# Optimization experiments

Measured on AMD Instinct MI355X. Metric: run time of the kernel, lower is better.

Reference implementation:

```python
import jax, jax.numpy as jnp
import numpy as np

SCORE_THRESH = 0.5
NMS_THRESH = 0.4
TOP_K = 1000  # fixed pre-NMS candidate budget (jit-safe replacement for boolean masking)
STRIDES = (8, 16, 32)
H, W = 2176, 3840


def _anchor_centers(fh, fw, stride):
    yv, xv = jnp.meshgrid(jnp.arange(fh), jnp.arange(fw), indexing='ij')
    return (jnp.stack([xv, yv], -1).reshape(-1, 2).astype(jnp.float32)) * stride  # [N,2]


def _decode_level(scores, bbox, kps, stride):
    fh, fw = H // stride, W // stride
    c = _anchor_centers(fh, fw, stride)                 # [N,2]
    s = jax.nn.sigmoid(scores.reshape(-1))              # [N]
    d = bbox.reshape(-1, 4) * stride                    # [N,4]
    boxes = jnp.concatenate([c - d[:, :2], c + d[:, 2:4]], axis=1)  # x1y1x2y2
    k = kps.reshape(-1, 5, 2) * stride + c[:, None, :]  # (x,y) pairs
    return s, boxes, k.reshape(-1, 10)


def _iou_matrix(b):
    area = (b[:, 2] - b[:, 0]) * (b[:, 3] - b[:, 1])
    lt = jnp.maximum(b[:, None, :2], b[None, :, :2])
    rb = jnp.minimum(b[:, None, 2:], b[None, :, 2:])
    wh = jnp.clip(rb - lt, 0.0)
    inter = wh[..., 0] * wh[..., 1]
    return inter / jnp.clip(area[:, None] + area[None, :] - inter, 1e-9)


def _nms_keep(iou, valid):
    n = iou.shape[0]
    ar = jnp.arange(n)

    def body(i, keep):
        sup = (iou[i] > NMS_THRESH) & (ar > i) & keep[i]
        return keep & ~sup

    return jax.lax.fori_loop(0, n, body, valid)


def reference(x, scores8, bbox8, kps8, scores16, bbox16, kps16, scores32, bbox32, kps32):
    levels = ((scores8, bbox8, kps8), (scores16, bbox16, kps16), (scores32, bbox32, kps32))
    ss, bs, ks = [], [], []
    for (s, b, k), stride in zip(levels, STRIDES):
        si, bi, ki = _decode_level(s, b, k, stride)
        ss.append(si); bs.append(bi); ks.append(ki)
    scores = jnp.concatenate(ss)   # [N_total]
    boxes = jnp.concatenate(bs)    # [N_total,4]
    kpss = jnp.concatenate(ks)     # [N_total,10]

    masked = jnp.where(scores > SCORE_THRESH, scores, -1.0)
    top_s, idx = jax.lax.top_k(masked, TOP_K)
    valid = top_s > SCORE_THRESH
    b = boxes[idx]
    k = kpss[idx]

    keep = jax.lax.stop_gradient(_nms_keep(_iou_matrix(b), valid))
    final_boxes = jnp.where(keep[:, None], b, 0.0)
    final_scores = jnp.where(keep, top_s, 0.0)
    final_kpss = jnp.where(keep[:, None], k, 0.0)
    return final_boxes, final_scores, final_kpss


def setup_inputs() -> dict:
    key = jax.random.key(0)
    ks = jax.random.split(key, 10)
    n8 = (H // 8) * (W // 8)
    n16 = (H // 16) * (W // 16)
    n32 = (H // 32) * (W // 32)
    return {
        'x': jax.random.normal(ks[0], (1, 3, H, W), jnp.float32),
        'scores8': jax.random.normal(ks[1], (1, n8, 1), jnp.float32),
        'bbox8': jax.random.uniform(ks[2], (1, n8, 4), jnp.float32),
        'kps8': jax.random.normal(ks[3], (1, n8, 10), jnp.float32),
        'scores16': jax.random.normal(ks[4], (1, n16, 1), jnp.float32),
        'bbox16': jax.random.uniform(ks[5], (1, n16, 4), jnp.float32),
        'kps16': jax.random.normal(ks[6], (1, n16, 10), jnp.float32),
        'scores32': jax.random.normal(ks[7], (1, n32, 1), jnp.float32),
        'bbox32': jax.random.uniform(ks[8], (1, n32, 4), jnp.float32),
        'kps32': jax.random.normal(ks[9], (1, n32, 10), jnp.float32),
    }
```

## Files before the change

### kernel.cpp

```cpp
#include <hip/hip_runtime.h>
#include <stdint.h>

typedef unsigned int u32;
typedef unsigned long long u64;

#define N8   130560
#define N16  32640
#define N32  8160
#define NTOT 171360
#define NTOT4 42840
#define TOPK 1000
#define NWORDS 16
#define NBINS 512
#define BUCKET_SCALE 85.25f
#define LIST_CAP 2016
#define CPB 32
#define HIST_BLKS 84
#define HIST_THR 512
#define CMP_BLKS 168
#define RANK_BLKS 63
#define IOU_BLKS 63
#define IOU_TASKS (TOPK * NWORDS)
#define NMS_CACHE 256
#define POISON 0xAAAAAAAAu


#define MI_CNT 0
#define MI_IOU 128
#define MI_ARR 256
#define MI_B   384
#define META_U32 512
#define META_ZERO 256

#define OFF_PART 0
#define OFF_META 86016
#define OFF_NZ   88064
#define OFF_LIST 88192
#define OFF_MASK 104320

__device__ __forceinline__ u32 ald32(const u32* p) {
  return __hip_atomic_load(p, __ATOMIC_RELAXED, __HIP_MEMORY_SCOPE_AGENT);
}
__device__ __forceinline__ u64 ald64(const u64* p) {
  return __hip_atomic_load(p, __ATOMIC_RELAXED, __HIP_MEMORY_SCOPE_AGENT);
}
__device__ __forceinline__ void ast32(u32* p, u32 v) {
  __hip_atomic_store(p, v, __ATOMIC_RELAXED, __HIP_MEMORY_SCOPE_AGENT);
}
__device__ __forceinline__ void ast64(u64* p, u64 v) {
  __hip_atomic_store(p, v, __ATOMIC_RELAXED, __HIP_MEMORY_SCOPE_AGENT);
}
__device__ __forceinline__ u32 normc(u32 v) {
  return v >= 0x80000000u ? v - POISON : v;
}
__device__ __forceinline__ bool arrive_last(u32* p, u32 total) {
  u32 old = __hip_atomic_fetch_add(p, 1u, __ATOMIC_RELAXED, __HIP_MEMORY_SCOPE_AGENT);
  if (normc(old) == total - 1u) { ast32(p, 0u); return true; }
  return false;
}

__device__ __forceinline__ u32 bucket_of(float x) {
  u32 b = (u32)(x * BUCKET_SCALE);
  return b > (NBINS - 1) ? (NBINS - 1) : b;
}

__device__ __forceinline__ float4 load_logit4(int v, const float* s8, const float* s16,
                                              const float* s32) {
  int e = v * 4;
  if (e < N8) return ((const float4*)s8)[v];
  if (e < N8 + N16) return ((const float4*)s16)[v - N8 / 4];
  return ((const float4*)s32)[v - (N8 + N16) / 4];
}

__device__ __forceinline__ bool iou_gt04(float4 a, float4 b) {
#pragma clang fp contract(off)
  float areaA = (a.z - a.x) * (a.w - a.y);
  float areaB = (b.z - b.x) * (b.w - b.y);
  float ltx = fmaxf(a.x, b.x);
  float lty = fmaxf(a.y, b.y);
  float rbx = fminf(a.z, b.z);
  float rby = fminf(a.w, b.w);
  float wx = rbx - ltx; wx = wx > 0.0f ? wx : 0.0f;
  float wy = rby - lty; wy = wy > 0.0f ? wy : 0.0f;
  float inter = wx * wy;
  float un = areaA + areaB - inter;
  un = un > 1e-9f ? un : 1e-9f;
  return (inter / un) > 0.4f;
}

__device__ __forceinline__ u64 valid_word(int w, u32 vcnt) {
  int lo = w * 64;
  if ((int)vcnt >= lo + 64) return ~0ull;
  if ((int)vcnt <= lo) return 0ull;
  return (1ull << (vcnt - (u32)lo)) - 1ull;
}

__global__ void __launch_bounds__(HIST_THR) k1_hist(
    const float* __restrict__ s8, const float* __restrict__ s16, const float* __restrict__ s32,
    u32* __restrict__ part, u32* meta, u64* __restrict__ nz) {
  __shared__ u32 lh[NBINS];
  __shared__ u32 csum[256];
  __shared__ int sLast;
  const int t = threadIdx.x, blk = blockIdx.x;
  lh[t < NBINS ? t : 0] = 0;
  __syncthreads();
  int v = blk * HIST_THR + t;
  if (v < NTOT4) {
    float4 x = load_logit4(v, s8, s16, s32);
    if (x.x > 0.0f) atomicAdd(&lh[bucket_of(x.x)], 1u);
    if (x.y > 0.0f) atomicAdd(&lh[bucket_of(x.y)], 1u);
    if (x.z > 0.0f) atomicAdd(&lh[bucket_of(x.z)], 1u);
    if (x.w > 0.0f) atomicAdd(&lh[bucket_of(x.w)], 1u);
  }
  __syncthreads();
  if (t < 256)
    ast32(&part[blk * 256 + t], lh[2 * t] | (lh[2 * t + 1] << 16));
  if (blk == 0) {
    if (t < META_ZERO) meta[t] = 0;
    if (t < NWORDS) nz[t] = 0ull;
  }
  __syncthreads();
  if (t == 0) sLast = arrive_last(&meta[MI_ARR], HIST_BLKS) ? 1 : 0;
  __syncthreads();
  if (!sLast) return;

  u32 lo = 0, hi = 0;
  if (t < 256) {
    int p = 0;
    for (; p + 4 <= HIST_BLKS; p += 4) {
      u32 a0 = ald32(&part[(p + 0) * 256 + t]);
      u32 a1 = ald32(&part[(p + 1) * 256 + t]);
      u32 a2 = ald32(&part[(p + 2) * 256 + t]);
      u32 a3 = ald32(&part[(p + 3) * 256 + t]);
      lo += (a0 & 0xFFFFu) + (a1 & 0xFFFFu) + (a2 & 0xFFFFu) + (a3 & 0xFFFFu);
      hi += (a0 >> 16) + (a1 >> 16) + (a2 >> 16) + (a3 >> 16);
    }
    for (; p < HIST_BLKS; ++p) {
      u32 a = ald32(&part[p * 256 + t]);
      lo += a & 0xFFFFu; hi += a >> 16;
    }
  }
  __syncthreads();
  if (t < 256) { lh[2 * t] = lo; lh[2 * t + 1] = hi; csum[t] = lo + hi; }
  __syncthreads();
  for (int off = 1; off < 256; off <<= 1) {
    u32 add = (t < 256 && t + off < 256) ? csum[t + off] : 0u;
    __syncthreads();
    if (t < 256) csum[t] += add;
    __syncthreads();
  }
  if (t == 0 && csum[0] < TOPK) meta[MI_B] = 0u;
  if (t < 256) {
    u32 above = (t < 255) ? csum[t + 1] : 0u;
    if (csum[t] >= TOPK && above < TOPK) {
      u32 cum = above + lh[2 * t + 1];
      meta[MI_B] = (cum >= TOPK) ? (u32)(2 * t + 1) : (u32)(2 * t);
    }
  }
}

__global__ void __launch_bounds__(256) k4_compact(
    const float* __restrict__ s8, const float* __restrict__ s16, const float* __restrict__ s32,
    u32* __restrict__ meta, u64* __restrict__ list) {
  __shared__ u32 sB, sBase;
  __shared__ u32 cnt16[16];
  const int t = threadIdx.x, blk = blockIdx.x;
  const int wave = t >> 6, lane = t & 63;
  const int v = blk * 256 + t;
  if (t == 0) sB = meta[MI_B];
  float4 x = make_float4(-1.f, -1.f, -1.f, -1.f);
  if (v < NTOT4) x = load_logit4(v, s8, s16, s32);
  __syncthreads();
  const u32 B = sB;
  float c[4] = {x.x, x.y, x.z, x.w};
  u32 win = 0;
#pragma unroll
  for (int j = 0; j < 4; ++j)
    if (c[j] > 0.0f && bucket_of(c[j]) >= B) win |= 1u << j;
  u32 wpos[4], wcnt[4];
#pragma unroll
  for (int j = 0; j < 4; ++j) {
    u64 bal = __ballot((win >> j) & 1u);
    wcnt[j] = (u32)__popcll(bal);
    wpos[j] = (u32)__popcll(bal & ((1ull << lane) - 1ull));
  }
  if (lane == 0) {
#pragma unroll
    for (int j = 0; j < 4; ++j) cnt16[wave * 4 + j] = wcnt[j];
  }
  __syncthreads();
  if (t == 0) {
    u32 tot = 0, pre[16];
#pragma unroll
    for (int k = 0; k < 16; ++k) { pre[k] = tot; tot += cnt16[k]; }
#pragma unroll
    for (int k = 0; k < 16; ++k) cnt16[k] = pre[k];
    sBase = tot ? atomicAdd(&meta[MI_CNT], tot) : 0u;
  }
  __syncthreads();
#pragma unroll
  for (int j = 0; j < 4; ++j) {
    if ((win >> j) & 1u) {
      u32 dst = sBase + cnt16[wave * 4 + j] + wpos[j];
      if (dst < LIST_CAP) {
        u32 idx = (u32)(v * 4 + j);
        list[dst] = ((u64)__float_as_uint(c[j]) << 32) | (u64)(~idx);
      }
    }
  }
}

__global__ void __launch_bounds__(256) k5_rank(
    const u32* __restrict__ meta, const u64* __restrict__ list,
    const float* __restrict__ bb8,  const float* __restrict__ kp8,
    const float* __restrict__ bb16, const float* __restrict__ kp16,
    const float* __restrict__ bb32, const float* __restrict__ kp32,
    float* __restrict__ out) {
  __shared__ __align__(16) u64 keys[LIST_CAP];
  __shared__ u32 rpart[256];
  __shared__ u32 sCnt;
  const int t = threadIdx.x, blk = blockIdx.x;
  if (t == 0) { u32 cc = meta[MI_CNT]; sCnt = cc > LIST_CAP ? LIST_CAP : cc; }
  __syncthreads();
  const u32 cnt = sCnt;
  for (int j = t; j < LIST_CAP; j += 256) keys[j] = (j < (int)cnt) ? list[j] : 0ull;
  __syncthreads();
  {
    const int ci = t & 31, sl = t >> 5;
    const int c = blk * CPB + ci;
    const int chunk = ((int)cnt + 7) >> 3;
    int lo = sl * chunk; if (lo > (int)cnt) lo = (int)cnt;
    int hi = lo + chunk; if (hi > (int)cnt) hi = (int)cnt;
    u64 my = keys[c];
    int r = 0, j = lo;
    for (; j + 4 <= hi; j += 4)
      r += (keys[j] > my) + (keys[j + 1] > my) + (keys[j + 2] > my) + (keys[j + 3] > my);
    for (; j < hi; ++j) r += (keys[j] > my);
    rpart[t] = (u32)r;
  }
  __syncthreads();
  if (t < CPB) {
    const int c = blk * CPB + t;
    if (c < (int)cnt) {
      int rank = 0;
#pragma unroll
      for (int q = 0; q < 8; ++q) rank += (int)rpart[t + 32 * q];
      if (rank < TOPK) {
        u64 my = keys[c];
        float lx = __uint_as_float((u32)(my >> 32));
        float sc = (float)(1.0 / (1.0 + exp(-(double)lx)));
        u32 idx = ~((u32)my);
        float4 box;
        float kv[10];
        int p, xq, yq;
        float st;
        const float *bb, *kp;
        if (idx < N8) {
          st = 8.f;  p = (int)idx;              xq = p % 480; yq = p / 480; bb = bb8;  kp = kp8;
        } else if (idx < N8 + N16) {
          st = 16.f; p = (int)idx - N8;         xq = p % 240; yq = p / 240; bb = bb16; kp = kp16;
        } else {
          st = 32.f; p = (int)idx - (N8 + N16); xq = p % 120; yq = p / 120; bb = bb32; kp = kp32;
        }
        float cx = (float)xq * st, cy = (float)yq * st;
        {
#pragma clang fp contract(off)
          float d0 = bb[4 * p + 0] * st;
          float d1 = bb[4 * p + 1] * st;
          float d2 = bb[4 * p + 2] * st;
          float d3 = bb[4 * p + 3] * st;
          box.x = cx - d0; box.y = cy - d1; box.z = cx + d2; box.w = cy + d3;
          for (int q = 0; q < 10; ++q)
            kv[q] = kp[10 * p + q] * st + ((q & 1) ? cy : cx);
        }
        ((float4*)out)[rank] = box;
        out[4000 + rank] = sc;
#pragma unroll
        for (int q = 0; q < 10; ++q) out[5000 + 10 * rank + q] = kv[q];
      }
    } else if (c < TOPK) {
      ((float4*)out)[c] = make_float4(0.f, 0.f, 0.f, 0.f);
      out[4000 + c] = 0.f;
#pragma unroll
      for (int q = 0; q < 10; ++q) out[5000 + 10 * c + q] = 0.f;
    }
  }
}

__global__ void __launch_bounds__(256) k67_iou_nms(
    u32* meta, u64* nzWords, u64* mask, float* out) {
  __shared__ __align__(16) char smem[36864];
  __shared__ int isLast;
  __shared__ u32 sPc[16], sOff17[17];
  __shared__ u64 sRem[NWORDS];
  const int t = threadIdx.x, blk = blockIdx.x;

  float4* boxes = (float4*)smem;
  for (int r = t; r < TOPK; r += 256) boxes[r] = ((const float4*)out)[r];
  __syncthreads();
  int task = blk * 256 + t;
  if (task < IOU_TASKS) {
    int w = task / 1000;
    int i = task - w * 1000;
    float4 a = boxes[i];
    int bse = w * 64;
    int jend = (bse + 64) < TOPK ? (bse + 64) : TOPK;
    u64 bits = 0;
    for (int j = bse; j < jend; ++j)
      if (j > i && iou_gt04(a, boxes[j])) bits |= 1ull << (j - bse);
    ast64(&mask[(u64)w * 1000 + i], bits);
    if (bits) atomicOr(&nzWords[i >> 6], 1ull << (i & 63));
  }
  __syncthreads();
  if (t == 0)
    isLast = (__hip_atomic_fetch_add(&meta[MI_IOU], 1u, __ATOMIC_RELAXED,
                                     __HIP_MEMORY_SCOPE_AGENT) == (u32)(IOU_BLKS - 1));
  __syncthreads();
  if (!isLast) return;

  u32 cc = meta[MI_CNT];
  if (cc > LIST_CAP) cc = LIST_CAP;
  const u32 vcnt = cc < TOPK ? cc : TOPK;
  u32* rows = (u32*)smem;
  u64* cache = (u64*)(smem + 4096);
  u64 nzv = 0;
  if (t < NWORDS) {
    nzv = ald64(&nzWords[t]) & valid_word(t, vcnt);
    sPc[t] = (u32)__popcll(nzv);
  }
  __syncthreads();
  if (t == 0) {
    u32 o = 0;
    for (int w = 0; w < NWORDS; ++w) { sOff17[w] = o; o += sPc[w]; }
    sOff17[16] = o;
  }
  __syncthreads();
  if (t < NWORDS) {
    u64 m = nzv;
    u32 o = sOff17[t];
    while (m) { int b = __builtin_ctzll(m); m &= m - 1; rows[o++] = (u32)(t * 64 + b); }
  }
  __syncthreads();
  const int S = (int)sOff17[16];
  const int Sc = S < NMS_CACHE ? S : NMS_CACHE;
  for (int idx = t; idx < Sc * NWORDS; idx += 256) {
    int s = idx >> 4, w = idx & 15;
    cache[s * NWORDS + w] = ald64(&mask[(u64)w * 1000 + rows[s]]);
  }
  __syncthreads();
  if (t < 64) {
    u64 remv = 0;
    for (int s = 0; s < S; ++s) {
      u32 row = rows[s];
      int c = (int)(row >> 6), b = (int)(row & 63);
      u64 remc = __shfl(remv, c);
      if (!((remc >> b) & 1ull)) {
        u64 m = 0;
        if (t < NWORDS)
          m = (s < NMS_CACHE) ? cache[s * NWORDS + t] : ald64(&mask[(u64)t * 1000 + row]);
        remv |= m;
      }
    }
    if (t < NWORDS) sRem[t] = valid_word(t, vcnt) & remv;
  }
  __syncthreads();
  for (int r = t; r < TOPK; r += 256) {
    if ((sRem[r >> 6] >> (r & 63)) & 1ull) {
      ((float4*)out)[r] = make_float4(0.f, 0.f, 0.f, 0.f);
      out[4000 + r] = 0.f;
#pragma unroll
      for (int q = 0; q < 10; ++q) out[5000 + 10 * r + q] = 0.f;
    }
  }
}

extern "C" void kernel_launch(void* const* d_in, const int* in_sizes, int n_in,
                              void* d_out, int out_size, void* d_ws, size_t ws_size,
                              hipStream_t stream) {
  const float* s8   = (const float*)d_in[1];
  const float* bb8  = (const float*)d_in[2];
  const float* kp8  = (const float*)d_in[3];
  const float* s16  = (const float*)d_in[4];
  const float* bb16 = (const float*)d_in[5];
  const float* kp16 = (const float*)d_in[6];
  const float* s32  = (const float*)d_in[7];
  const float* bb32 = (const float*)d_in[8];
  const float* kp32 = (const float*)d_in[9];

  char* ws = (char*)d_ws;
  u32* part    = (u32*)(ws + OFF_PART);
  u32* meta    = (u32*)(ws + OFF_META);
  u64* nzWords = (u64*)(ws + OFF_NZ);
  u64* list    = (u64*)(ws + OFF_LIST);
  u64* mask    = (u64*)(ws + OFF_MASK);
  float* out   = (float*)d_out;

  k1_hist<<<HIST_BLKS, HIST_THR, 0, stream>>>(s8, s16, s32, part, meta, nzWords);
  k4_compact<<<CMP_BLKS, 256, 0, stream>>>(s8, s16, s32, meta, list);
  k5_rank<<<RANK_BLKS, 256, 0, stream>>>(meta, list, bb8, kp8, bb16, kp16, bb32, kp32, out);
  k67_iou_nms<<<IOU_BLKS, 256, 0, stream>>>(meta, nzWords, mask, out);
}
```

Measured before the change: 169.7 us.

## Precompute per-block compaction offsets in histogram kernel, drop global atomic counter

The histogram kernel now uses 42 blocks that each cover 1024 float4s, caches the per-block partial histograms in LDS, and in the last block computes each block's count of winners above threshold bucket B together with exclusive prefix offsets. The compaction kernel uses the same 42-block partition and writes to those precomputed bases, replacing the global atomicAdd on a shared counter. This also makes list order deterministic. The IoU kernel moves to 32 blocks of 512 threads. The trade-offs are fewer blocks in the streaming kernels and more serial work in the last histogram block.

```diff
diff --git a/kernel.cpp b/kernel.cpp
--- a/kernel.cpp
+++ b/kernel.cpp
@@ -15,28 +15,29 @@
 #define BUCKET_SCALE 85.25f
 #define LIST_CAP 2016
 #define CPB 32
-#define HIST_BLKS 84
-#define HIST_THR 512
-#define CMP_BLKS 168
+#define NB1 42
+#define THR1 512
 #define RANK_BLKS 63
-#define IOU_BLKS 63
+#define IOU_BLKS 32
+#define IOU_THR 512
 #define IOU_TASKS (TOPK * NWORDS)
 #define NMS_CACHE 256
 #define POISON 0xAAAAAAAAu
 
 
-#define MI_CNT 0
-#define MI_IOU 128
-#define MI_ARR 256
-#define MI_B   384
+#define MI_IOU  0
+#define MI_ARR  128
+#define MI_B    256
+#define MI_TOT  257
+#define MI_BASE 258
 #define META_U32 512
-#define META_ZERO 256
+#define META_ZERO 128
 
 #define OFF_PART 0
-#define OFF_META 86016
-#define OFF_NZ   88064
-#define OFF_LIST 88192
-#define OFF_MASK 104320
+#define OFF_META 43008
+#define OFF_NZ   45056
+#define OFF_LIST 45184
+#define OFF_MASK 61312
 
 __device__ __forceinline__ u32 ald32(const u32* p) {
   return __hip_atomic_load(p, __ATOMIC_RELAXED, __HIP_MEMORY_SCOPE_AGENT);
@@ -95,18 +96,31 @@
   return (1ull << (vcnt - (u32)lo)) - 1ull;
 }
 
-__global__ void __launch_bounds__(HIST_THR) k1_hist(
+__global__ void __launch_bounds__(THR1) k1_hist(
     const float* __restrict__ s8, const float* __restrict__ s16, const float* __restrict__ s32,
     u32* __restrict__ part, u32* meta, u64* __restrict__ nz) {
   __shared__ u32 lh[NBINS];
+  __shared__ u32 ldsp[NB1 * 256];
   __shared__ u32 csum[256];
+  __shared__ u32 redlo[THR1], redhi[THR1];
+  __shared__ u32 red8[64][8];
+  __shared__ u32 base42[NB1 + 1];
+  __shared__ u32 sB2;
   __shared__ int sLast;
   const int t = threadIdx.x, blk = blockIdx.x;
-  lh[t < NBINS ? t : 0] = 0;
-  __syncthreads();
-  int v = blk * HIST_THR + t;
-  if (v < NTOT4) {
-    float4 x = load_logit4(v, s8, s16, s32);
+
+  if (t < NBINS) lh[t] = 0;
+  __syncthreads();
+  const int v0 = blk * 1024 + t, v1 = v0 + 512;
+  if (v0 < NTOT4) {
+    float4 x = load_logit4(v0, s8, s16, s32);
+    if (x.x > 0.0f) atomicAdd(&lh[bucket_of(x.x)], 1u);
+    if (x.y > 0.0f) atomicAdd(&lh[bucket_of(x.y)], 1u);
+    if (x.z > 0.0f) atomicAdd(&lh[bucket_of(x.z)], 1u);
+    if (x.w > 0.0f) atomicAdd(&lh[bucket_of(x.w)], 1u);
+  }
+  if (v1 < NTOT4) {
+    float4 x = load_logit4(v1, s8, s16, s32);
     if (x.x > 0.0f) atomicAdd(&lh[bucket_of(x.x)], 1u);
     if (x.y > 0.0f) atomicAdd(&lh[bucket_of(x.y)], 1u);
     if (x.z > 0.0f) atomicAdd(&lh[bucket_of(x.z)], 1u);
@@ -120,28 +134,27 @@
     if (t < NWORDS) nz[t] = 0ull;
   }
   __syncthreads();
-  if (t == 0) sLast = arrive_last(&meta[MI_ARR], HIST_BLKS) ? 1 : 0;
+  if (t == 0) sLast = arrive_last(&meta[MI_ARR], NB1) ? 1 : 0;
   __syncthreads();
   if (!sLast) return;
 
-  u32 lo = 0, hi = 0;
+  {
+    const u32 b = (u32)(t & 255);
+    u32 lo = 0, hi = 0;
+    for (int p = t >> 8; p < NB1; p += 2) {
+      u32 w = ald32(&part[p * 256 + b]);
+      ldsp[p * 256 + b] = w;
+      lo += w & 0xFFFFu; hi += w >> 16;
+    }
+    redlo[t] = lo; redhi[t] = hi;
+  }
+  __syncthreads();
+  u32 glo = 0, ghi = 0;
   if (t < 256) {
-    int p = 0;
-    for (; p + 4 <= HIST_BLKS; p += 4) {
-      u32 a0 = ald32(&part[(p + 0) * 256 + t]);
-      u32 a1 = ald32(&part[(p + 1) * 256 + t]);
-      u32 a2 = ald32(&part[(p + 2) * 256 + t]);
-      u32 a3 = ald32(&part[(p + 3) * 256 + t]);
-      lo += (a0 & 0xFFFFu) + (a1 & 0xFFFFu) + (a2 & 0xFFFFu) + (a3 & 0xFFFFu);
-      hi += (a0 >> 16) + (a1 >> 16) + (a2 >> 16) + (a3 >> 16);
-    }
-    for (; p < HIST_BLKS; ++p) {
-      u32 a = ald32(&part[p * 256 + t]);
-      lo += a & 0xFFFFu; hi += a >> 16;
-    }
-  }
-  __syncthreads();
-  if (t < 256) { lh[2 * t] = lo; lh[2 * t + 1] = hi; csum[t] = lo + hi; }
+    glo = redlo[t] + redlo[t + 256];
+    ghi = redhi[t] + redhi[t + 256];
+    csum[t] = glo + ghi;
+  }
   __syncthreads();
   for (int off = 1; off < 256; off <<= 1) {
     u32 add = (t < 256 && t + off < 256) ? csum[t + off] : 0u;
@@ -149,61 +162,86 @@
     if (t < 256) csum[t] += add;
     __syncthreads();
   }
-  if (t == 0 && csum[0] < TOPK) meta[MI_B] = 0u;
+  if (t == 0 && csum[0] < TOPK) sB2 = 0u;
   if (t < 256) {
     u32 above = (t < 255) ? csum[t + 1] : 0u;
-    if (csum[t] >= TOPK && above < TOPK) {
-      u32 cum = above + lh[2 * t + 1];
-      meta[MI_B] = (cum >= TOPK) ? (u32)(2 * t + 1) : (u32)(2 * t);
-    }
-  }
-}
-
-__global__ void __launch_bounds__(256) k4_compact(
+    if (csum[t] >= TOPK && above < TOPK)
+      sB2 = (above + ghi >= TOPK) ? (u32)(2 * t + 1) : (u32)(2 * t);
+  }
+  __syncthreads();
+  const u32 B = sB2;
+
+  {
+    const int g = t >> 3, l = t & 7;
+    u32 acc = 0;
+    if (g < NB1) {
+      const int wB = (int)(B >> 1);
+      for (int w = l * 32; w < l * 32 + 32; ++w) {
+        if (w < wB) continue;
+        u32 pv = ldsp[g * 256 + w];
+        u32 c = pv >> 16;
+        if (w > wB || !(B & 1u)) c += pv & 0xFFFFu;
+        acc += c;
+      }
+      red8[g][l] = acc;
+    }
+  }
+  __syncthreads();
+  if (t == 0) {
+    u32 run = 0;
+    for (int p = 0; p < NB1; ++p) {
+      u32 c = red8[p][0] + red8[p][1] + red8[p][2] + red8[p][3]
+            + red8[p][4] + red8[p][5] + red8[p][6] + red8[p][7];
+      base42[p] = run; run += c;
+    }
+    base42[NB1] = run;
+    meta[MI_B] = B;
+    meta[MI_TOT] = run > LIST_CAP ? LIST_CAP : run;
+  }
+  __syncthreads();
+  if (t < NB1) meta[MI_BASE + t] = base42[t];
+}
+
+__global__ void __launch_bounds__(THR1) k4_compact(
     const float* __restrict__ s8, const float* __restrict__ s16, const float* __restrict__ s32,
-    u32* __restrict__ meta, u64* __restrict__ list) {
+    const u32* __restrict__ meta, u64* __restrict__ list) {
   __shared__ u32 sB, sBase;
-  __shared__ u32 cnt16[16];
+  __shared__ u32 cnt64[64];
   const int t = threadIdx.x, blk = blockIdx.x;
   const int wave = t >> 6, lane = t & 63;
-  const int v = blk * 256 + t;
-  if (t == 0) sB = meta[MI_B];
-  float4 x = make_float4(-1.f, -1.f, -1.f, -1.f);
-  if (v < NTOT4) x = load_logit4(v, s8, s16, s32);
+  if (t == 0) { sB = meta[MI_B]; sBase = meta[MI_BASE + blk]; }
+  const int v0 = blk * 1024 + t, v1 = v0 + 512;
+  float4 x0 = make_float4(-1.f, -1.f, -1.f, -1.f), x1 = x0;
+  if (v0 < NTOT4) x0 = load_logit4(v0, s8, s16, s32);
+  if (v1 < NTOT4) x1 = load_logit4(v1, s8, s16, s32);
   __syncthreads();
   const u32 B = sB;
-  float c[4] = {x.x, x.y, x.z, x.w};
+  float c[8] = {x0.x, x0.y, x0.z, x0.w, x1.x, x1.y, x1.z, x1.w};
   u32 win = 0;
 #pragma unroll
-  for (int j = 0; j < 4; ++j)
+  for (int j = 0; j < 8; ++j)
     if (c[j] > 0.0f && bucket_of(c[j]) >= B) win |= 1u << j;
-  u32 wpos[4], wcnt[4];
-#pragma unroll
-  for (int j = 0; j < 4; ++j) {
+  u32 wpos[8];
+#pragma unroll
+  for (int j = 0; j < 8; ++j) {
     u64 bal = __ballot((win >> j) & 1u);
-    wcnt[j] = (u32)__popcll(bal);
+    if (lane == 0) cnt64[wave * 8 + j] = (u32)__popcll(bal);
     wpos[j] = (u32)__popcll(bal & ((1ull << lane) - 1ull));
   }
-  if (lane == 0) {
-#pragma unroll
-    for (int j = 0; j < 4; ++j) cnt16[wave * 4 + j] = wcnt[j];
-  }
   __syncthreads();
   if (t == 0) {
-    u32 tot = 0, pre[16];
-#pragma unroll
-    for (int k = 0; k < 16; ++k) { pre[k] = tot; tot += cnt16[k]; }
-#pragma unroll
-    for (int k = 0; k < 16; ++k) cnt16[k] = pre[k];
-    sBase = tot ? atomicAdd(&meta[MI_CNT], tot) : 0u;
-  }
-  __syncthreads();
-#pragma unroll
-  for (int j = 0; j < 4; ++j) {
+    u32 run = 0;
+#pragma unroll
+    for (int k = 0; k < 64; ++k) { u32 x = cnt64[k]; cnt64[k] = run; run += x; }
+  }
+  __syncthreads();
+  const u32 base = sBase;
+#pragma unroll
+  for (int j = 0; j < 8; ++j) {
     if ((win >> j) & 1u) {
-      u32 dst = sBase + cnt16[wave * 4 + j] + wpos[j];
+      u32 dst = base + cnt64[wave * 8 + j] + wpos[j];
       if (dst < LIST_CAP) {
-        u32 idx = (u32)(v * 4 + j);
+        u32 idx = (u32)(((j < 4) ? v0 : v1) * 4 + (j & 3));
         list[dst] = ((u64)__float_as_uint(c[j]) << 32) | (u64)(~idx);
       }
     }
@@ -220,7 +258,7 @@
   __shared__ u32 rpart[256];
   __shared__ u32 sCnt;
   const int t = threadIdx.x, blk = blockIdx.x;
-  if (t == 0) { u32 cc = meta[MI_CNT]; sCnt = cc > LIST_CAP ? LIST_CAP : cc; }
+  if (t == 0) sCnt = meta[MI_TOT];
   __syncthreads();
   const u32 cnt = sCnt;
   for (int j = t; j < LIST_CAP; j += 256) keys[j] = (j < (int)cnt) ? list[j] : 0ull;
@@ -287,7 +325,7 @@
   }
 }
 
-__global__ void __launch_bounds__(256) k67_iou_nms(
+__global__ void __launch_bounds__(IOU_THR) k67_iou_nms(
     u32* meta, u64* nzWords, u64* mask, float* out) {
   __shared__ __align__(16) char smem[36864];
   __shared__ int isLast;
@@ -296,9 +334,9 @@
   const int t = threadIdx.x, blk = blockIdx.x;
 
   float4* boxes = (float4*)smem;
-  for (int r = t; r < TOPK; r += 256) boxes[r] = ((const float4*)out)[r];
-  __syncthreads();
-  int task = blk * 256 + t;
+  for (int r = t; r < TOPK; r += IOU_THR) boxes[r] = ((const float4*)out)[r];
+  __syncthreads();
+  int task = blk * IOU_THR + t;
   if (task < IOU_TASKS) {
     int w = task / 1000;
     int i = task - w * 1000;
@@ -318,8 +356,7 @@
   __syncthreads();
   if (!isLast) return;
 
-  u32 cc = meta[MI_CNT];
-  if (cc > LIST_CAP) cc = LIST_CAP;
+  u32 cc = meta[MI_TOT];
   const u32 vcnt = cc < TOPK ? cc : TOPK;
   u32* rows = (u32*)smem;
   u64* cache = (u64*)(smem + 4096);
@@ -343,7 +380,7 @@
   __syncthreads();
   const int S = (int)sOff17[16];
   const int Sc = S < NMS_CACHE ? S : NMS_CACHE;
-  for (int idx = t; idx < Sc * NWORDS; idx += 256) {
+  for (int idx = t; idx < Sc * NWORDS; idx += IOU_THR) {
     int s = idx >> 4, w = idx & 15;
     cache[s * NWORDS + w] = ald64(&mask[(u64)w * 1000 + rows[s]]);
   }
@@ -364,7 +401,7 @@
     if (t < NWORDS) sRem[t] = valid_word(t, vcnt) & remv;
   }
   __syncthreads();
-  for (int r = t; r < TOPK; r += 256) {
+  for (int r = t; r < TOPK; r += IOU_THR) {
     if ((sRem[r >> 6] >> (r & 63)) & 1ull) {
       ((float4*)out)[r] = make_float4(0.f, 0.f, 0.f, 0.f);
       out[4000 + r] = 0.f;
@@ -395,8 +432,8 @@
   u64* mask    = (u64*)(ws + OFF_MASK);
   float* out   = (float*)d_out;
 
-  k1_hist<<<HIST_BLKS, HIST_THR, 0, stream>>>(s8, s16, s32, part, meta, nzWords);
-  k4_compact<<<CMP_BLKS, 256, 0, stream>>>(s8, s16, s32, meta, list);
+  k1_hist<<<NB1, THR1, 0, stream>>>(s8, s16, s32, part, meta, nzWords);
+  k4_compact<<<NB1, THR1, 0, stream>>>(s8, s16, s32, meta, list);
   k5_rank<<<RANK_BLKS, 256, 0, stream>>>(meta, list, bb8, kp8, bb16, kp16, bb32, kp32, out);
-  k67_iou_nms<<<IOU_BLKS, 256, 0, stream>>>(meta, nzWords, mask, out);
-}
+  k67_iou_nms<<<IOU_BLKS, IOU_THR, 0, stream>>>(meta, nzWords, mask, out);
+}
```

New measurement: 174.9 us. 3.1% more time.

## Replace last-block histogram reduction with redundant per-block reduction in compact kernel

Applied to the files above, without the earlier changes.

The histogram kernel no longer uses an atomic arrive counter to elect a last block that reduces the partial histograms and picks the threshold bucket. Instead, every compact block re-reduces all 84 partial histograms from global memory, runs a prefix scan in shared memory and computes the bucket threshold locally. This removes the serialized tail where one block does the reduction after all others finish, along with the atomic arrival logic. In exchange, every compact block reads about 86 KB of partials and runs a scan before it can compact.

```diff
diff --git a/kernel.cpp b/kernel.cpp
--- a/kernel.cpp
+++ b/kernel.cpp
@@ -22,41 +22,23 @@
 #define IOU_BLKS 63
 #define IOU_TASKS (TOPK * NWORDS)
 #define NMS_CACHE 256
-#define POISON 0xAAAAAAAAu
 
 
 #define MI_CNT 0
 #define MI_IOU 128
-#define MI_ARR 256
-#define MI_B   384
-#define META_U32 512
-#define META_ZERO 256
+#define META_U32 256
 
 #define OFF_PART 0
 #define OFF_META 86016
-#define OFF_NZ   88064
-#define OFF_LIST 88192
-#define OFF_MASK 104320
-
-__device__ __forceinline__ u32 ald32(const u32* p) {
-  return __hip_atomic_load(p, __ATOMIC_RELAXED, __HIP_MEMORY_SCOPE_AGENT);
-}
+#define OFF_NZ   87040
+#define OFF_LIST 87168
+#define OFF_MASK 103296
+
 __device__ __forceinline__ u64 ald64(const u64* p) {
   return __hip_atomic_load(p, __ATOMIC_RELAXED, __HIP_MEMORY_SCOPE_AGENT);
 }
-__device__ __forceinline__ void ast32(u32* p, u32 v) {
-  __hip_atomic_store(p, v, __ATOMIC_RELAXED, __HIP_MEMORY_SCOPE_AGENT);
-}
 __device__ __forceinline__ void ast64(u64* p, u64 v) {
   __hip_atomic_store(p, v, __ATOMIC_RELAXED, __HIP_MEMORY_SCOPE_AGENT);
-}
-__device__ __forceinline__ u32 normc(u32 v) {
-  return v >= 0x80000000u ? v - POISON : v;
-}
-__device__ __forceinline__ bool arrive_last(u32* p, u32 total) {
-  u32 old = __hip_atomic_fetch_add(p, 1u, __ATOMIC_RELAXED, __HIP_MEMORY_SCOPE_AGENT);
-  if (normc(old) == total - 1u) { ast32(p, 0u); return true; }
-  return false;
 }
 
 __device__ __forceinline__ u32 bucket_of(float x) {
@@ -97,12 +79,10 @@
 
 __global__ void __launch_bounds__(HIST_THR) k1_hist(
     const float* __restrict__ s8, const float* __restrict__ s16, const float* __restrict__ s32,
-    u32* __restrict__ part, u32* meta, u64* __restrict__ nz) {
+    u32* __restrict__ part, u32* __restrict__ meta, u64* __restrict__ nz) {
   __shared__ u32 lh[NBINS];
-  __shared__ u32 csum[256];
-  __shared__ int sLast;
   const int t = threadIdx.x, blk = blockIdx.x;
-  lh[t < NBINS ? t : 0] = 0;
+  if (t < NBINS) lh[t] = 0;
   __syncthreads();
   int v = blk * HIST_THR + t;
   if (v < NTOT4) {
@@ -114,63 +94,55 @@
   }
   __syncthreads();
   if (t < 256)
-    ast32(&part[blk * 256 + t], lh[2 * t] | (lh[2 * t + 1] << 16));
+    part[blk * 256 + t] = lh[2 * t] | (lh[2 * t + 1] << 16);
   if (blk == 0) {
-    if (t < META_ZERO) meta[t] = 0;
+    if (t < META_U32) meta[t] = 0;
     if (t < NWORDS) nz[t] = 0ull;
-  }
-  __syncthreads();
-  if (t == 0) sLast = arrive_last(&meta[MI_ARR], HIST_BLKS) ? 1 : 0;
-  __syncthreads();
-  if (!sLast) return;
-
-  u32 lo = 0, hi = 0;
-  if (t < 256) {
-    int p = 0;
-    for (; p + 4 <= HIST_BLKS; p += 4) {
-      u32 a0 = ald32(&part[(p + 0) * 256 + t]);
-      u32 a1 = ald32(&part[(p + 1) * 256 + t]);
-      u32 a2 = ald32(&part[(p + 2) * 256 + t]);
-      u32 a3 = ald32(&part[(p + 3) * 256 + t]);
-      lo += (a0 & 0xFFFFu) + (a1 & 0xFFFFu) + (a2 & 0xFFFFu) + (a3 & 0xFFFFu);
-      hi += (a0 >> 16) + (a1 >> 16) + (a2 >> 16) + (a3 >> 16);
-    }
-    for (; p < HIST_BLKS; ++p) {
-      u32 a = ald32(&part[p * 256 + t]);
-      lo += a & 0xFFFFu; hi += a >> 16;
-    }
-  }
-  __syncthreads();
-  if (t < 256) { lh[2 * t] = lo; lh[2 * t + 1] = hi; csum[t] = lo + hi; }
-  __syncthreads();
-  for (int off = 1; off < 256; off <<= 1) {
-    u32 add = (t < 256 && t + off < 256) ? csum[t + off] : 0u;
-    __syncthreads();
-    if (t < 256) csum[t] += add;
-    __syncthreads();
-  }
-  if (t == 0 && csum[0] < TOPK) meta[MI_B] = 0u;
-  if (t < 256) {
-    u32 above = (t < 255) ? csum[t + 1] : 0u;
-    if (csum[t] >= TOPK && above < TOPK) {
-      u32 cum = above + lh[2 * t + 1];
-      meta[MI_B] = (cum >= TOPK) ? (u32)(2 * t + 1) : (u32)(2 * t);
-    }
   }
 }
 
 __global__ void __launch_bounds__(256) k4_compact(
     const float* __restrict__ s8, const float* __restrict__ s16, const float* __restrict__ s32,
-    u32* __restrict__ meta, u64* __restrict__ list) {
+    const u32* __restrict__ part, u32* __restrict__ meta, u64* __restrict__ list) {
+  __shared__ u32 csum[256];
   __shared__ u32 sB, sBase;
   __shared__ u32 cnt16[16];
   const int t = threadIdx.x, blk = blockIdx.x;
   const int wave = t >> 6, lane = t & 63;
   const int v = blk * 256 + t;
-  if (t == 0) sB = meta[MI_B];
   float4 x = make_float4(-1.f, -1.f, -1.f, -1.f);
   if (v < NTOT4) x = load_logit4(v, s8, s16, s32);
-  __syncthreads();
+
+  u32 lo = 0, hi = 0;
+  {
+    int p = 0;
+    for (; p + 4 <= HIST_BLKS; p += 4) {
+      u32 a0 = part[(p + 0) * 256 + t];
+      u32 a1 = part[(p + 1) * 256 + t];
+      u32 a2 = part[(p + 2) * 256 + t];
+      u32 a3 = part[(p + 3) * 256 + t];
+      lo += (a0 & 0xFFFFu) + (a1 & 0xFFFFu) + (a2 & 0xFFFFu) + (a3 & 0xFFFFu);
+      hi += (a0 >> 16) + (a1 >> 16) + (a2 >> 16) + (a3 >> 16);
+    }
+    for (; p < HIST_BLKS; ++p) {
+      u32 a = part[p * 256 + t];
+      lo += a & 0xFFFFu; hi += a >> 16;
+    }
+  }
+  csum[t] = lo + hi;
+  __syncthreads();
+  for (int off = 1; off < 256; off <<= 1) {
+    u32 add = (t + off < 256) ? csum[t + off] : 0u;
+    __syncthreads();
+    csum[t] += add;
+    __syncthreads();
+  }
+  u32 above = (t < 255) ? csum[t + 1] : 0u;
+  if (t == 0 && csum[0] < TOPK) sB = 0u;
+  if (csum[t] >= TOPK && above < TOPK)
+    sB = (above + hi >= TOPK) ? (u32)(2 * t + 1) : (u32)(2 * t);
+  __syncthreads();
+
   const u32 B = sB;
   float c[4] = {x.x, x.y, x.z, x.w};
   u32 win = 0;
@@ -396,7 +368,7 @@
   float* out   = (float*)d_out;
 
   k1_hist<<<HIST_BLKS, HIST_THR, 0, stream>>>(s8, s16, s32, part, meta, nzWords);
-  k4_compact<<<CMP_BLKS, 256, 0, stream>>>(s8, s16, s32, meta, list);
+  k4_compact<<<CMP_BLKS, 256, 0, stream>>>(s8, s16, s32, part, meta, list);
   k5_rank<<<RANK_BLKS, 256, 0, stream>>>(meta, list, bb8, kp8, bb16, kp16, bb32, kp32, out);
   k67_iou_nms<<<IOU_BLKS, 256, 0, stream>>>(meta, nzWords, mask, out);
 }
```

Result: no change. 166.7 us, median of 2 (-1.8%).
